# Performance work log

Hardware: AMD Instinct MI355X
Metric: run time of the kernel (lower is better)

## Reference

```python
import jax, jax.numpy as jnp
import numpy as np

N = 50000
E = 800000
IN_C, HID, HEADS, CLS = 128, 64, 5, 40
NEG_SLOPE = 0.2


def gat_conv(h, src, dst, W, a_src, a_dst, bias, heads, out_c, concat):
    n = h.shape[0]
    hp = (h @ W).reshape(n, heads, out_c)            # [N,H,C]
    a_s = jnp.sum(hp * a_src, axis=-1)               # [N,H]
    a_d = jnp.sum(hp * a_dst, axis=-1)               # [N,H]
    e = jax.nn.leaky_relu(a_s[src] + a_d[dst], NEG_SLOPE)  # [Etot,H]
    m = jax.ops.segment_max(e, dst, num_segments=n)  # segment softmax over dst
    e = jnp.exp(e - m[dst])
    s = jax.ops.segment_sum(e, dst, num_segments=n)
    alpha = e / (s[dst] + 1e-16)                     # [Etot,H]
    msg = hp[src] * alpha[:, :, None]                # [Etot,H,C]
    out = jax.ops.segment_sum(msg, dst, num_segments=n)
    if concat:
        out = out.reshape(n, heads * out_c)
    else:
        out = out.mean(axis=1)
    return out + bias


def setup_inputs() -> dict:
    key = jax.random.key(0)
    ks = jax.random.split(key, 12)
    x = jax.random.normal(ks[0], (N, IN_C), dtype=jnp.float32)
    edge_index = jax.random.randint(ks[1], (2, E), 0, N, dtype=jnp.int64)
    g = 0.1
    return {
        "x": x,
        "edge_index": edge_index,
        "emb_W": jax.random.normal(ks[2], (IN_C, HID), jnp.float32) * g,
        "emb_b": jnp.zeros((HID,), jnp.float32),
        "W1": jax.random.normal(ks[3], (HID, HEADS * HID), jnp.float32) * g,
        "att_src1": jax.random.normal(ks[4], (HEADS, HID), jnp.float32) * g,
        "att_dst1": jax.random.normal(ks[5], (HEADS, HID), jnp.float32) * g,
        "b1": jnp.zeros((HEADS * HID,), jnp.float32),
        "W2": jax.random.normal(ks[6], (HEADS * HID, HEADS * CLS), jnp.float32) * g,
        "att_src2": jax.random.normal(ks[7], (HEADS, CLS), jnp.float32) * g,
        "att_dst2": jax.random.normal(ks[8], (HEADS, CLS), jnp.float32) * g,
        "b2": jnp.zeros((CLS,), jnp.float32),
    }


def reference(x, edge_index, emb_W, emb_b, W1, att_src1, att_dst1, b1,
              W2, att_src2, att_dst2, b2):
    n = x.shape[0]
    loops = jnp.arange(n, dtype=edge_index.dtype)
    src = jnp.concatenate([edge_index[0], loops])  # PyG adds self-loops
    dst = jnp.concatenate([edge_index[1], loops])
    h = x @ emb_W + emb_b
    emb = h
    # dropout skipped (eval mode)
    h = jax.nn.elu(gat_conv(h, src, dst, W1, att_src1, att_dst1, b1, HEADS, HID, True))
    h = gat_conv(h, src, dst, W2, att_src2, att_dst2, b2, HEADS, CLS, False)
    return emb, jax.nn.log_softmax(h, axis=1)
```

## Files before the change

### kernel.cpp

```cpp
#include <hip/hip_runtime.h>
#include <math.h>

constexpr int N_NODES = 50000;
constexpr int E_EDGES = 800000;
constexpr int ETOT    = E_EDGES + N_NODES;
constexpr int IN_C    = 128;
constexpr int HID     = 64;
constexpr int HEADS   = 5;
constexpr int CLS     = 40;
constexpr int SLOTW   = 96;
constexpr float NEG_SLOPE = 0.2f;

typedef __attribute__((ext_vector_type(8))) short short8;
typedef __attribute__((ext_vector_type(4))) float float4v;
typedef __attribute__((ext_vector_type(2))) float f32x2;

__device__ __forceinline__ float lrelu(float v) {
    return v > 0.f ? v : NEG_SLOPE * v;
}
__device__ __forceinline__ float bf2f(unsigned short u) {
    return __uint_as_float(((unsigned)u) << 16);
}
__device__ __forceinline__ f32x2 bfp2f(unsigned u) {
    f32x2 r;
    r.x = __uint_as_float(u << 16);
    r.y = __uint_as_float(u & 0xFFFF0000u);
    return r;
}
__device__ __forceinline__ unsigned short f2bf(float f) {
    unsigned u = __float_as_uint(f);
    return (unsigned short)((u + 0x7fffu + ((u >> 16) & 1u)) >> 16);
}

__device__ __forceinline__ void pack_one(const float* __restrict__ B,
                                         unsigned short* __restrict__ Bp,
                                         int N, int KS, int t)
{
    int lane = t & 63;
    int f = (t >> 6) & 3;
    int rest = t >> 8;
    int ks = rest % KS;
    int nt = rest / KS;
    int n = nt * 64 + f * 16 + (lane & 15);
    int kbase = ks * 32 + (lane >> 4) * 8;
    unsigned short vals[8];
    #pragma unroll
    for (int j = 0; j < 8; j++) {
        float v = (n < N) ? B[(long)(kbase + j) * N + n] : 0.f;
        vals[j] = f2bf(v);
    }
    *(ushort4*)(Bp + (long)t * 8)     = make_ushort4(vals[0], vals[1], vals[2], vals[3]);
    *(ushort4*)(Bp + (long)t * 8 + 4) = make_ushort4(vals[4], vals[5], vals[6], vals[7]);
}

__global__ void build_graph(const int* __restrict__ ei, int* __restrict__ cnt,
                            unsigned short* __restrict__ slots,
                            const float* __restrict__ W0, const float* __restrict__ W1,
                            const float* __restrict__ W2,
                            const float* __restrict__ att1s, const float* __restrict__ att1d,
                            const float* __restrict__ att2s, const float* __restrict__ att2d,
                            unsigned short* __restrict__ Bp0,
                            unsigned short* __restrict__ Bp1,
                            unsigned short* __restrict__ Bp2,
                            float* __restrict__ u1s, float* __restrict__ u1d,
                            unsigned short* __restrict__ Bs)
{
    int t = blockIdx.x * blockDim.x + threadIdx.x;
    if (t < 13824) {
        if (t < 1024)      pack_one(W0, Bp0, 64,  4,  t);
        else if (t < 3584) pack_one(W1, Bp1, 320, 2,  t - 1024);
        else               pack_one(W2, Bp2, 200, 10, t - 3584);
    } else if (t < 14464) {
        int i = t - 13824;
        bool isd = i >= 320;
        int j = isd ? i - 320 : i;
        int h = j >> 6, k = j & 63;
        const float* att = isd ? att1d : att1s;
        float sum = 0.f;
        for (int c = 0; c < 64; c++)
            sum += W1[k * 320 + h * 64 + c] * att[h * 64 + c];
        (isd ? u1d : u1s)[j] = sum;
    } else if (t < 15104) {
        int i = t - 14464;
        int lane = i & 63, ks = i >> 6;
        int n = lane & 15, kq = lane >> 4;
        unsigned short vals[8];
        #pragma unroll
        for (int j = 0; j < 8; j++) {
            int k = ks * 32 + kq * 8 + j;
            float sum = 0.f;
            if (n < 5) {
                for (int c = 0; c < 40; c++)
                    sum += W2[k * 200 + n * 40 + c] * att2s[n * 40 + c];
            } else if (n >= 8 && n < 13) {
                int h = n - 8;
                for (int c = 0; c < 40; c++)
                    sum += W2[k * 200 + h * 40 + c] * att2d[h * 40 + c];
            }
            vals[j] = f2bf(sum);
        }
        *(ushort4*)(Bs + (long)i * 8)     = make_ushort4(vals[0], vals[1], vals[2], vals[3]);
        *(ushort4*)(Bs + (long)i * 8 + 4) = make_ushort4(vals[4], vals[5], vals[6], vals[7]);
    }
    if (t >= ETOT) return;
    int s, d;
    if (t < E_EDGES) { s = ei[t]; d = ei[E_EDGES + t]; }
    else             { s = d = t - E_EDGES; }
    int pos = atomicAdd(&cnt[d], 1);
    if (pos < SLOTW) slots[d * SLOTW + pos] = (unsigned short)s;
}

__global__ __launch_bounds__(256) void gemm_mfma_emb(
    const float* __restrict__ A, const unsigned short* __restrict__ Bp,
    const float* __restrict__ bias,
    const float* __restrict__ u1s, const float* __restrict__ u1d,
    float* __restrict__ Cf, unsigned short* __restrict__ Cb,
    float* __restrict__ asd, int M)
{
    const int K = 128, KS = 4;
    const int w = threadIdx.x >> 6, lane = threadIdx.x & 63;
    const int cl = lane & 15, kq = lane >> 4;
    int rowA = blockIdx.x * 64 + w * 16 + cl;
    if (rowA >= M) rowA = M - 1;
    const float* ap = A + (long)rowA * K + kq * 8;
    const unsigned short* bp = Bp + lane * 8;
    float4v acc[4] = {};
    #pragma unroll
    for (int ks = 0; ks < KS; ks++) {
        float4 u0 = *(const float4*)(ap + ks * 32);
        float4 u1 = *(const float4*)(ap + ks * 32 + 4);
        short8 a;
        a[0] = f2bf(u0.x); a[1] = f2bf(u0.y); a[2] = f2bf(u0.z); a[3] = f2bf(u0.w);
        a[4] = f2bf(u1.x); a[5] = f2bf(u1.y); a[6] = f2bf(u1.z); a[7] = f2bf(u1.w);
        #pragma unroll
        for (int f = 0; f < 4; f++) {
            short8 b = *(const short8*)(bp + ks * 2048 + f * 512);
            acc[f] = __builtin_amdgcn_mfma_f32_16x16x32_bf16(a, b, acc[f], 0, 0, 0);
        }
    }
    int rbase = blockIdx.x * 64 + w * 16 + kq * 4;
    float bc4[4];
    #pragma unroll
    for (int f = 0; f < 4; f++) {
        int col = f * 16 + cl;
        float bc = bias[col];
        bc4[f] = bc;
        #pragma unroll
        for (int r = 0; r < 4; r++) {
            int row = rbase + r;
            if (row < M) {
                float v = acc[f][r] + bc;
                Cf[(long)row * 64 + col] = v;
                Cb[(long)row * 64 + col] = f2bf(v);
            }
        }
    }
    #pragma unroll
    for (int h = 0; h < HEADS; h++) {
        float us[4], ud[4];
        #pragma unroll
        for (int f = 0; f < 4; f++) {
            us[f] = u1s[h * 64 + f * 16 + cl];
            ud[f] = u1d[h * 64 + f * 16 + cl];
        }
        #pragma unroll
        for (int r = 0; r < 4; r++) {
            float ps = 0.f, pd = 0.f;
            #pragma unroll
            for (int f = 0; f < 4; f++) {
                float v = acc[f][r] + bc4[f];
                ps += v * us[f];
                pd += v * ud[f];
            }
            #pragma unroll
            for (int off = 1; off < 16; off <<= 1) {
                ps += __shfl_xor(ps, off);
                pd += __shfl_xor(pd, off);
            }
            int row = rbase + r;
            if (cl == 0 && row < M) {
                asd[row * 16 + h]     = ps;
                asd[row * 16 + 8 + h] = pd;
            }
        }
    }
}

__global__ __launch_bounds__(256) void aggr1_new(
    const int* __restrict__ cnt, const unsigned short* __restrict__ slots,
    const float* __restrict__ asd,
    const unsigned short* __restrict__ emb, unsigned short* __restrict__ e_out)
{
    __shared__ float alph[4][64 * 8];
    int wid = (blockIdx.x * blockDim.x + threadIdx.x) >> 6;
    int w = threadIdx.x >> 6;
    int lane = threadIdx.x & 63;
    if (wid >= N_NODES) return;
    int deg = cnt[wid];
    if (deg > SLOTW) deg = SLOTW;
    const unsigned short* myslot = slots + wid * SLOTW;

    float adh[HEADS];
    #pragma unroll
    for (int h = 0; h < HEADS; h++) adh[h] = asd[wid * 16 + 8 + h];

    const char* embB = (const char*)emb;

    if (deg <= 64) {
        bool has = lane < deg;
        int s = has ? (int)myslot[lane] : 0;
        int rowoff = s * 128;
        float4 s4 = *(const float4*)(asd + s * 16);
        float  s5 = asd[s * 16 + 4];
        float v[HEADS], mx[HEADS], sm[HEADS];
        v[0] = has ? lrelu(s4.x + adh[0]) : -1e30f;
        v[1] = has ? lrelu(s4.y + adh[1]) : -1e30f;
        v[2] = has ? lrelu(s4.z + adh[2]) : -1e30f;
        v[3] = has ? lrelu(s4.w + adh[3]) : -1e30f;
        v[4] = has ? lrelu(s5   + adh[4]) : -1e30f;
        #pragma unroll
        for (int h = 0; h < HEADS; h++) mx[h] = v[h];
        if (deg <= 32) {
            #pragma unroll
            for (int h = 0; h < HEADS; h++)
                #pragma unroll
                for (int off = 16; off; off >>= 1)
                    mx[h] = fmaxf(mx[h], __shfl_xor(mx[h], off));
        } else {
            #pragma unroll
            for (int h = 0; h < HEADS; h++)
                #pragma unroll
                for (int off = 32; off; off >>= 1)
                    mx[h] = fmaxf(mx[h], __shfl_xor(mx[h], off));
        }
        #pragma unroll
        for (int h = 0; h < HEADS; h++) {
            float e = has ? __expf(v[h] - mx[h]) : 0.f;
            v[h] = e;
            sm[h] = e;
        }
        if (deg <= 32) {
            #pragma unroll
            for (int h = 0; h < HEADS; h++)
                #pragma unroll
                for (int off = 16; off; off >>= 1)
                    sm[h] += __shfl_xor(sm[h], off);
        } else {
            #pragma unroll
            for (int h = 0; h < HEADS; h++)
                #pragma unroll
                for (int off = 32; off; off >>= 1)
                    sm[h] += __shfl_xor(sm[h], off);
        }
        #pragma unroll
        for (int h = 0; h < HEADS; h++)
            alph[w][lane * 8 + h] = v[h] / (sm[h] + 1e-16f);

        const int g = lane >> 4, cl16 = lane & 15;
        f32x2 av[HEADS][2] = {};
        int nE8 = (deg + 7) & ~7;
        for (int i = 0; i < nE8; i += 8) {
            int e0 = i + g, e1 = i + 4 + g;
            int off0 = __shfl(rowoff, e0);
            int off1 = __shfl(rowoff, e1);
            uint2 q0 = *(const uint2*)(embB + off0 + cl16 * 8);
            uint2 q1 = *(const uint2*)(embB + off1 + cl16 * 8);
            float4 b0 = *(const float4*)&alph[w][e0 * 8];
            float  b4 = alph[w][e0 * 8 + 4];
            float4 c0 = *(const float4*)&alph[w][e1 * 8];
            float  c4 = alph[w][e1 * 8 + 4];
            f32x2 f0a = bfp2f(q0.x), f0b = bfp2f(q0.y);
            f32x2 f1a = bfp2f(q1.x), f1b = bfp2f(q1.y);
            av[0][0] += f0a * b0.x; av[0][1] += f0b * b0.x;
            av[1][0] += f0a * b0.y; av[1][1] += f0b * b0.y;
            av[2][0] += f0a * b0.z; av[2][1] += f0b * b0.z;
            av[3][0] += f0a * b0.w; av[3][1] += f0b * b0.w;
            av[4][0] += f0a * b4;   av[4][1] += f0b * b4;
            av[0][0] += f1a * c0.x; av[0][1] += f1b * c0.x;
            av[1][0] += f1a * c0.y; av[1][1] += f1b * c0.y;
            av[2][0] += f1a * c0.z; av[2][1] += f1b * c0.z;
            av[3][0] += f1a * c0.w; av[3][1] += f1b * c0.w;
            av[4][0] += f1a * c4;   av[4][1] += f1b * c4;
        }
        #pragma unroll
        for (int h = 0; h < HEADS; h++)
            #pragma unroll
            for (int p = 0; p < 2; p++) {
                float tx = av[h][p].x, ty = av[h][p].y;
                tx += __shfl_xor(tx, 16); tx += __shfl_xor(tx, 32);
                ty += __shfl_xor(ty, 16); ty += __shfl_xor(ty, 32);
                av[h][p].x = tx; av[h][p].y = ty;
            }
        if (g == 0) {
            #pragma unroll
            for (int h = 0; h < HEADS; h++) {
                ushort4 o = make_ushort4(f2bf(av[h][0].x), f2bf(av[h][0].y),
                                         f2bf(av[h][1].x), f2bf(av[h][1].y));
                *(ushort4*)(e_out + (long)wid * 320 + h * 64 + cl16 * 4) = o;
            }
        }
    } else {
        float acc[HEADS] = {};
        float mx[HEADS], inv[HEADS], sm[HEADS] = {};
        #pragma unroll
        for (int h = 0; h < HEADS; h++) mx[h] = -1e30f;
        for (int e = lane; e < deg; e += 64) {
            int s = myslot[e];
            #pragma unroll
            for (int h = 0; h < HEADS; h++)
                mx[h] = fmaxf(mx[h], lrelu(asd[s * 16 + h] + adh[h]));
        }
        #pragma unroll
        for (int h = 0; h < HEADS; h++)
            #pragma unroll
            for (int off = 32; off; off >>= 1)
                mx[h] = fmaxf(mx[h], __shfl_xor(mx[h], off));
        for (int e = lane; e < deg; e += 64) {
            int s = myslot[e];
            #pragma unroll
            for (int h = 0; h < HEADS; h++)
                sm[h] += __expf(lrelu(asd[s * 16 + h] + adh[h]) - mx[h]);
        }
        #pragma unroll
        for (int h = 0; h < HEADS; h++) {
            #pragma unroll
            for (int off = 32; off; off >>= 1)
                sm[h] += __shfl_xor(sm[h], off);
            inv[h] = 1.f / (sm[h] + 1e-16f);
        }
        for (int e = 0; e < deg; e++) {
            int s0 = myslot[e];
            float fv = bf2f(*(const unsigned short*)(embB + s0 * 128 + lane * 2));
            #pragma unroll
            for (int h = 0; h < HEADS; h++) {
                float a0 = __expf(lrelu(asd[s0 * 16 + h] + adh[h]) - mx[h]) * inv[h];
                acc[h] += fv * a0;
            }
        }
        #pragma unroll
        for (int h = 0; h < HEADS; h++)
            e_out[(long)wid * 320 + h * 64 + lane] = f2bf(acc[h]);
    }
}

__global__ __launch_bounds__(256, 5) void gemm_mix_l2(
    const unsigned short* __restrict__ A, const unsigned short* __restrict__ Bp1,
    const unsigned short* __restrict__ Bp2, const float* __restrict__ bias,
    const unsigned short* __restrict__ Bs,
    unsigned short* __restrict__ hp2, float* __restrict__ asd, int M)
{
    constexpr int LDP = 328;
    __shared__ unsigned short tile[32 * LDP];
    const int wid = threadIdx.x >> 6, lane = threadIdx.x & 63;
    const int band = wid >> 1, half = wid & 1;
    const int cl = lane & 15, kq = lane >> 4;
    int rowA = blockIdx.x * 32 + band * 16 + cl;
    if (rowA >= M) rowA = M - 1;
    const unsigned short* ap = A + (long)rowA * 320;
    const unsigned short* bp1 = Bp1 + lane * 8;

    const int rbase = blockIdx.x * 32 + band * 16 + kq * 4;
    const int lrow = band * 16 + kq * 4;

    if (half == 0) {
        float4v acc[12] = {};
        #pragma unroll
        for (int i = 0; i < 3; i++)
            #pragma unroll
            for (int ks = 0; ks < 2; ks++) {
                short8 a = *(const short8*)(ap + i * 64 + ks * 32 + kq * 8);
                #pragma unroll
                for (int f = 0; f < 4; f++) {
                    short8 b = *(const short8*)(bp1 + (i * 2 + ks) * 2048 + f * 512);
                    acc[i * 4 + f] =
                        __builtin_amdgcn_mfma_f32_16x16x32_bf16(a, b, acc[i * 4 + f], 0, 0, 0);
                }
            }
        #pragma unroll
        for (int i = 0; i < 3; i++)
            #pragma unroll
            for (int f = 0; f < 4; f++) {
                int col = i * 64 + f * 16 + cl;
                float bc = bias[col];
                #pragma unroll
                for (int r = 0; r < 4; r++) {
                    float v = acc[i * 4 + f][r] + bc;
                    v = v > 0.f ? v : __expf(v) - 1.f;
                    tile[(lrow + r) * LDP + col] = f2bf(v);
                }
            }
    } else {
        float4v acc[8] = {};
        #pragma unroll
        for (int i = 0; i < 2; i++)
            #pragma unroll
            for (int ks = 0; ks < 2; ks++) {
                short8 a = *(const short8*)(ap + (3 + i) * 64 + ks * 32 + kq * 8);
                #pragma unroll
                for (int f = 0; f < 4; f++) {
                    short8 b = *(const short8*)(bp1 + ((3 + i) * 2 + ks) * 2048 + f * 512);
                    acc[i * 4 + f] =
                        __builtin_amdgcn_mfma_f32_16x16x32_bf16(a, b, acc[i * 4 + f], 0, 0, 0);
                }
            }
        #pragma unroll
        for (int i = 0; i < 2; i++)
            #pragma unroll
            for (int f = 0; f < 4; f++) {
                int col = (3 + i) * 64 + f * 16 + cl;
                float bc = bias[col];
                #pragma unroll
                for (int r = 0; r < 4; r++) {
                    float v = acc[i * 4 + f][r] + bc;
                    v = v > 0.f ? v : __expf(v) - 1.f;
                    tile[(lrow + r) * LDP + col] = f2bf(v);
                }
            }
    }
    __syncthreads();

    const unsigned short* arow = tile + (band * 16 + cl) * LDP;
    const unsigned short* bp2 = Bp2 + lane * 8;
    const unsigned short* bs  = Bs + lane * 8;
    float4v acc2[8] = {};
    float4v accs = {};
    #pragma unroll
    for (int ks = 0; ks < 10; ks++) {
        short8 a2 = *(const short8*)(arow + ks * 32 + kq * 8);
        if (half == 0) {
            short8 b = *(const short8*)(bs + ks * 512);
            accs = __builtin_amdgcn_mfma_f32_16x16x32_bf16(a2, b, accs, 0, 0, 0);
        }
        #pragma unroll
        for (int nt2 = 0; nt2 < 2; nt2++)
            #pragma unroll
            for (int f = 0; f < 4; f++) {
                short8 b = *(const short8*)(bp2 + (((half * 2 + nt2) * 10 + ks) * 2048) + f * 512);
                acc2[nt2 * 4 + f] =
                    __builtin_amdgcn_mfma_f32_16x16x32_bf16(a2, b, acc2[nt2 * 4 + f], 0, 0, 0);
            }
    }
    if (half == 0) {
        #pragma unroll
        for (int r = 0; r < 4; r++) {
            int row = rbase + r;
            if (row < M) asd[row * 16 + cl] = accs[r];
        }
    }
    #pragma unroll
    for (int nt2 = 0; nt2 < 2; nt2++)
        #pragma unroll
        for (int f = 0; f < 4; f++) {
            int col = (half * 2 + nt2) * 64 + f * 16 + cl;
            if (col >= 200) continue;
            #pragma unroll
            for (int r = 0; r < 4; r++) {
                int row = rbase + r;
                if (row < M) hp2[(long)row * 200 + col] = f2bf(acc2[nt2 * 4 + f][r]);
            }
        }
}

__global__ __launch_bounds__(256) void aggr2_fused(
    const int* __restrict__ cnt, const unsigned short* __restrict__ slots,
    const float* __restrict__ asd,
    const unsigned short* __restrict__ hp, const float* __restrict__ bias,
    float* __restrict__ out)
{
    __shared__ float alph[4][320];
    int wid = (blockIdx.x * blockDim.x + threadIdx.x) >> 6;
    int w = threadIdx.x >> 6;
    int lane = threadIdx.x & 63;
    if (wid >= N_NODES) return;
    int deg = cnt[wid];
    if (deg > SLOTW) deg = SLOTW;
    const unsigned short* myslot = slots + wid * SLOTW;

    float adh[HEADS];
    #pragma unroll
    for (int h = 0; h < HEADS; h++) adh[h] = asd[wid * 16 + 8 + h];

    const bool act = lane < 50;
    const int ch4 = lane * 4;
    const int hq  = act ? lane / 10 : 0;
    const char* hpB = (const char*)hp;
    f32x2 acc01 = {0.f, 0.f}, acc23 = {0.f, 0.f};

    if (deg <= 64) {
        bool has = lane < deg;
        int s = has ? (int)myslot[lane] : 0;
        int rowoff = s * 400;
        float4 s4 = *(const float4*)(asd + s * 16);
        float  s5 = asd[s * 16 + 4];
        float v[HEADS], mx[HEADS], sm[HEADS];
        v[0] = has ? lrelu(s4.x + adh[0]) : -1e30f;
        v[1] = has ? lrelu(s4.y + adh[1]) : -1e30f;
        v[2] = has ? lrelu(s4.z + adh[2]) : -1e30f;
        v[3] = has ? lrelu(s4.w + adh[3]) : -1e30f;
        v[4] = has ? lrelu(s5   + adh[4]) : -1e30f;
        #pragma unroll
        for (int h = 0; h < HEADS; h++) mx[h] = v[h];
        if (deg <= 32) {
            #pragma unroll
            for (int h = 0; h < HEADS; h++)
                #pragma unroll
                for (int off = 16; off; off >>= 1)
                    mx[h] = fmaxf(mx[h], __shfl_xor(mx[h], off));
        } else {
            #pragma unroll
            for (int h = 0; h < HEADS; h++)
                #pragma unroll
                for (int off = 32; off; off >>= 1)
                    mx[h] = fmaxf(mx[h], __shfl_xor(mx[h], off));
        }
        #pragma unroll
        for (int h = 0; h < HEADS; h++) {
            float e = has ? __expf(v[h] - mx[h]) : 0.f;
            v[h] = e;
            sm[h] = e;
        }
        if (deg <= 32) {
            #pragma unroll
            for (int h = 0; h < HEADS; h++)
                #pragma unroll
                for (int off = 16; off; off >>= 1)
                    sm[h] += __shfl_xor(sm[h], off);
        } else {
            #pragma unroll
            for (int h = 0; h < HEADS; h++)
                #pragma unroll
                for (int off = 32; off; off >>= 1)
                    sm[h] += __shfl_xor(sm[h], off);
        }
        if (has) {
            #pragma unroll
            for (int h = 0; h < HEADS; h++)
                alph[w][lane * 5 + h] = 0.2f * v[h] / (sm[h] + 1e-16f);
        }
        int i = 0;
        for (; i + 7 < deg; i += 8) {
            uint2 q[8]; float a[8];
            #pragma unroll
            for (int k = 0; k < 8; k++) {
                int off = __shfl(rowoff, i + k);
                q[k] = act ? *(const uint2*)(hpB + off + ch4 * 2)
                           : make_uint2(0u, 0u);
                a[k] = alph[w][(i + k) * 5 + hq];
            }
            #pragma unroll
            for (int k = 0; k < 8; k++) {
                f32x2 fa = bfp2f(q[k].x), fb = bfp2f(q[k].y);
                acc01 += fa * a[k];
                acc23 += fb * a[k];
            }
        }
        for (; i < deg; i++) {
            int off = __shfl(rowoff, i);
            if (act) {
                uint2 q0 = *(const uint2*)(hpB + off + ch4 * 2);
                float a0 = alph[w][i * 5 + hq];
                f32x2 fa = bfp2f(q0.x), fb = bfp2f(q0.y);
                acc01 += fa * a0;
                acc23 += fb * a0;
            }
        }
    } else {
        float mx[HEADS], inv[HEADS], sm[HEADS] = {};
        #pragma unroll
        for (int h = 0; h < HEADS; h++) mx[h] = -1e30f;
        for (int e = lane; e < deg; e += 64) {
            int s = myslot[e];
            #pragma unroll
            for (int h = 0; h < HEADS; h++)
                mx[h] = fmaxf(mx[h], lrelu(asd[s * 16 + h] + adh[h]));
        }
        #pragma unroll
        for (int h = 0; h < HEADS; h++)
            #pragma unroll
            for (int off = 32; off; off >>= 1)
                mx[h] = fmaxf(mx[h], __shfl_xor(mx[h], off));
        for (int e = lane; e < deg; e += 64) {
            int s = myslot[e];
            #pragma unroll
            for (int h = 0; h < HEADS; h++)
                sm[h] += __expf(lrelu(asd[s * 16 + h] + adh[h]) - mx[h]);
        }
        #pragma unroll
        for (int h = 0; h < HEADS; h++) {
            #pragma unroll
            for (int off = 32; off; off >>= 1)
                sm[h] += __shfl_xor(sm[h], off);
            inv[h] = 0.2f / (sm[h] + 1e-16f);
        }
        for (int e = 0; e < deg; e++) {
            int s0 = myslot[e];
            if (act) {
                uint2 q0 = *(const uint2*)(hpB + s0 * 400 + ch4 * 2);
                float a0 = __expf(lrelu(asd[s0 * 16 + hq] + adh[hq]) - mx[hq]) * inv[hq];
                f32x2 fa = bfp2f(q0.x), fb = bfp2f(q0.y);
                acc01 += fa * a0;
                acc23 += fb * a0;
            }
        }
    }

    float acc0 = acc01.x, acc1 = acc01.y, acc2 = acc23.x, acc3 = acc23.y;
    float r0 = acc0, r1 = acc1, r2 = acc2, r3 = acc3;
    #pragma unroll
    for (int h5 = 1; h5 < 5; h5++) {
        int sl = (lane + 10 * h5) & 63;
        r0 += __shfl(acc0, sl);
        r1 += __shfl(acc1, sl);
        r2 += __shfl(acc2, sl);
        r3 += __shfl(acc3, sl);
    }

    float vb0 = -1e30f, vb1 = -1e30f, vb2 = -1e30f, vb3 = -1e30f;
    if (lane < 10) {
        vb0 = r0 + bias[ch4 + 0];
        vb1 = r1 + bias[ch4 + 1];
        vb2 = r2 + bias[ch4 + 2];
        vb3 = r3 + bias[ch4 + 3];
    }
    float mxv = fmaxf(fmaxf(vb0, vb1), fmaxf(vb2, vb3));
    #pragma unroll
    for (int off = 32; off; off >>= 1)
        mxv = fmaxf(mxv, __shfl_xor(mxv, off));
    float sme = 0.f;
    if (lane < 10)
        sme = __expf(vb0 - mxv) + __expf(vb1 - mxv) +
              __expf(vb2 - mxv) + __expf(vb3 - mxv);
    #pragma unroll
    for (int off = 32; off; off >>= 1)
        sme += __shfl_xor(sme, off);
    float ls = mxv + __logf(sme);
    if (lane < 10) {
        float4 o = make_float4(vb0 - ls, vb1 - ls, vb2 - ls, vb3 - ls);
        *(float4*)(out + (long)wid * CLS + ch4) = o;
    }
}

extern "C" void kernel_launch(void* const* d_in, const int* in_sizes, int n_in,
                              void* d_out, int out_size, void* d_ws, size_t ws_size,
                              hipStream_t stream)
{
    const float* x     = (const float*)d_in[0];
    const int*   ei    = (const int*)d_in[1];
    const float* emb_W = (const float*)d_in[2];
    const float* emb_b = (const float*)d_in[3];
    const float* W1    = (const float*)d_in[4];
    const float* as1   = (const float*)d_in[5];
    const float* ad1   = (const float*)d_in[6];
    const float* b1    = (const float*)d_in[7];
    const float* W2    = (const float*)d_in[8];
    const float* as2   = (const float*)d_in[9];
    const float* ad2   = (const float*)d_in[10];
    const float* b2    = (const float*)d_in[11];

    float* out_emb = (float*)d_out;
    float* out_cls = (float*)d_out + (size_t)N_NODES * HID;

    char* ws = (char*)d_ws;
    unsigned short* e_agg  = (unsigned short*)(ws);
    unsigned short* hp2b   = (unsigned short*)(ws + 32000000);
    float*          asd1   = (float*)(ws + 52000000);
    float*          asd2   = (float*)(ws + 55200000);
    unsigned short* embb   = (unsigned short*)(ws + 64000000);
    unsigned short* Bp0    = (unsigned short*)(ws + 74400000);
    unsigned short* Bp1    = (unsigned short*)(ws + 74500000);
    unsigned short* Bp2    = (unsigned short*)(ws + 74600000);
    float*          u1s    = (float*)(ws + 74800000);
    float*          u1d    = (float*)(ws + 74810000);
    unsigned short* Bs     = (unsigned short*)(ws + 74820000);
    int*            cnt    = (int*)(ws + 74840000);
    unsigned short* slots  = (unsigned short*)(ws + 75100000);

    const dim3 blk(256);
    const int eb   = (ETOT + 255) / 256;
    const int nb4  = (N_NODES + 3) / 4;
    const int mgrid  = (N_NODES + 63) / 64;
    const int mgrid2 = (N_NODES + 31) / 32;

    hipMemsetAsync(cnt, 0, (size_t)N_NODES * 4, stream);
    build_graph<<<eb, blk, 0, stream>>>(ei, cnt, slots, emb_W, W1, W2,
                                        as1, ad1, as2, ad2,
                                        Bp0, Bp1, Bp2, u1s, u1d, Bs);

    gemm_mfma_emb<<<mgrid, blk, 0, stream>>>(x, Bp0, emb_b, u1s, u1d,
                                             out_emb, embb, asd1, N_NODES);

    aggr1_new<<<nb4, blk, 0, stream>>>(cnt, slots, asd1, embb, e_agg);

    gemm_mix_l2<<<mgrid2, blk, 0, stream>>>(e_agg, Bp1, Bp2, b1, Bs,
                                            hp2b, asd2, N_NODES);

    aggr2_fused<<<nb4, blk, 0, stream>>>(cnt, slots, asd2, hp2b, b2, out_cls);
}
```

Before: 343.0 us.

## Split weight packing out and co-launch edge scatter with embedding GEMM

Moves weight packing into its own small kernel. The edge-to-slot scatter now runs as extra blocks inside the embedding GEMM launch, so the atomic-heavy scatter and the MFMA GEMM can overlap on the device instead of running one after the other. This adds one kernel launch, and the GEMM blocks now compete with the scatter for memory bandwidth within the same grid.

Measured after the change: 350.1 us. 2.1% more time.

```diff
diff --git a/kernel.cpp b/kernel.cpp
--- a/kernel.cpp
+++ b/kernel.cpp
@@ -53,17 +53,15 @@
     *(ushort4*)(Bp + (long)t * 8 + 4) = make_ushort4(vals[4], vals[5], vals[6], vals[7]);
 }
 
-__global__ void build_graph(const int* __restrict__ ei, int* __restrict__ cnt,
-                            unsigned short* __restrict__ slots,
-                            const float* __restrict__ W0, const float* __restrict__ W1,
-                            const float* __restrict__ W2,
-                            const float* __restrict__ att1s, const float* __restrict__ att1d,
-                            const float* __restrict__ att2s, const float* __restrict__ att2d,
-                            unsigned short* __restrict__ Bp0,
-                            unsigned short* __restrict__ Bp1,
-                            unsigned short* __restrict__ Bp2,
-                            float* __restrict__ u1s, float* __restrict__ u1d,
-                            unsigned short* __restrict__ Bs)
+__global__ void pack_weights(const float* __restrict__ W0, const float* __restrict__ W1,
+                             const float* __restrict__ W2,
+                             const float* __restrict__ att1s, const float* __restrict__ att1d,
+                             const float* __restrict__ att2s, const float* __restrict__ att2d,
+                             unsigned short* __restrict__ Bp0,
+                             unsigned short* __restrict__ Bp1,
+                             unsigned short* __restrict__ Bp2,
+                             float* __restrict__ u1s, float* __restrict__ u1d,
+                             unsigned short* __restrict__ Bs)
 {
     int t = blockIdx.x * blockDim.x + threadIdx.x;
     if (t < 13824) {
@@ -102,25 +100,32 @@
         *(ushort4*)(Bs + (long)i * 8)     = make_ushort4(vals[0], vals[1], vals[2], vals[3]);
         *(ushort4*)(Bs + (long)i * 8 + 4) = make_ushort4(vals[4], vals[5], vals[6], vals[7]);
     }
-    if (t >= ETOT) return;
-    int s, d;
-    if (t < E_EDGES) { s = ei[t]; d = ei[E_EDGES + t]; }
-    else             { s = d = t - E_EDGES; }
-    int pos = atomicAdd(&cnt[d], 1);
-    if (pos < SLOTW) slots[d * SLOTW + pos] = (unsigned short)s;
-}
-
-__global__ __launch_bounds__(256) void gemm_mfma_emb(
+}
+
+__global__ __launch_bounds__(256) void emb_scatter_fused(
     const float* __restrict__ A, const unsigned short* __restrict__ Bp,
     const float* __restrict__ bias,
     const float* __restrict__ u1s, const float* __restrict__ u1d,
     float* __restrict__ Cf, unsigned short* __restrict__ Cb,
-    float* __restrict__ asd, int M)
+    float* __restrict__ asd, int M,
+    const int* __restrict__ ei, int* __restrict__ cnt,
+    unsigned short* __restrict__ slots, int nScat)
 {
+    if ((int)blockIdx.x < nScat) {
+        int t = blockIdx.x * 256 + threadIdx.x;
+        if (t >= ETOT) return;
+        int s, d;
+        if (t < E_EDGES) { s = ei[t]; d = ei[E_EDGES + t]; }
+        else             { s = d = t - E_EDGES; }
+        int pos = atomicAdd(&cnt[d], 1);
+        if (pos < SLOTW) slots[d * SLOTW + pos] = (unsigned short)s;
+        return;
+    }
+    const int gb = blockIdx.x - nScat;
     const int K = 128, KS = 4;
     const int w = threadIdx.x >> 6, lane = threadIdx.x & 63;
     const int cl = lane & 15, kq = lane >> 4;
-    int rowA = blockIdx.x * 64 + w * 16 + cl;
+    int rowA = gb * 64 + w * 16 + cl;
     if (rowA >= M) rowA = M - 1;
     const float* ap = A + (long)rowA * K + kq * 8;
     const unsigned short* bp = Bp + lane * 8;
@@ -138,7 +143,7 @@
             acc[f] = __builtin_amdgcn_mfma_f32_16x16x32_bf16(a, b, acc[f], 0, 0, 0);
         }
     }
-    int rbase = blockIdx.x * 64 + w * 16 + kq * 4;
+    int rbase = gb * 64 + w * 16 + kq * 4;
     float bc4[4];
     #pragma unroll
     for (int f = 0; f < 4; f++) {
@@ -676,18 +681,19 @@
     unsigned short* slots  = (unsigned short*)(ws + 75100000);
 
     const dim3 blk(256);
-    const int eb   = (ETOT + 255) / 256;
     const int nb4  = (N_NODES + 3) / 4;
     const int mgrid  = (N_NODES + 63) / 64;
     const int mgrid2 = (N_NODES + 31) / 32;
+    const int nScat  = (ETOT + 255) / 256;
+    const int pgrid  = (15104 + 255) / 256;
 
     hipMemsetAsync(cnt, 0, (size_t)N_NODES * 4, stream);
-    build_graph<<<eb, blk, 0, stream>>>(ei, cnt, slots, emb_W, W1, W2,
-                                        as1, ad1, as2, ad2,
-                                        Bp0, Bp1, Bp2, u1s, u1d, Bs);
-
-    gemm_mfma_emb<<<mgrid, blk, 0, stream>>>(x, Bp0, emb_b, u1s, u1d,
-                                             out_emb, embb, asd1, N_NODES);
+    pack_weights<<<pgrid, blk, 0, stream>>>(emb_W, W1, W2, as1, ad1, as2, ad2,
+                                            Bp0, Bp1, Bp2, u1s, u1d, Bs);
+
+    emb_scatter_fused<<<nScat + mgrid, blk, 0, stream>>>(
+        x, Bp0, emb_b, u1s, u1d, out_emb, embb, asd1, N_NODES,
+        ei, cnt, slots, nScat);
 
     aggr1_new<<<nb4, blk, 0, stream>>>(cnt, slots, asd1, embb, e_agg);
 
```
